# Optimization experiments

Hardware: AMD Instinct MI355X
Metric: run time of the kernel (lower is better)

Reference implementation:

```python
import jax, jax.numpy as jnp
import numpy as np

RADIUS = 0.1
WEIGHT = 0.2
MATMUL_NORM = False


def setup_inputs() -> dict:
    key = jax.random.key(0)
    k1, k2, k3, k4, k5 = jax.random.split(key, 5)
    S, B, Ck, Cv, H, W = 8, 2, 64, 64, 64, 64
    return {
        "memory_keys": jax.random.normal(k1, (S, B, Ck, H, W), jnp.float32),
        "memory_values": jax.random.normal(k2, (S, B, Cv, H, W), jnp.float32),
        "query_query": jax.random.normal(k3, (B, Ck, H, W), jnp.float32),
        "disparity": jax.random.normal(k4, (B, 1, H, W), jnp.float32),
        "sequence_index": jax.random.randint(k5, (B, S, 2), 0, 10, jnp.int32),
    }


def reference(memory_keys, memory_values, query_query, disparity, sequence_index):
    S, B, Ck, H, W = memory_keys.shape
    Cv = memory_values.shape[2]
    HW, SHW = H * W, S * H * W

    # keys: [B, Ck, S*H*W]; queries: [B, H*W, Ck]
    keys = jnp.transpose(memory_keys, (1, 2, 0, 3, 4)).reshape(B, Ck, SHW)
    q = jnp.transpose(query_query.reshape(B, Ck, HW), (0, 2, 1))

    # disparity-based additive mask, vectorized over frames
    weight = WEIGHT / S / H / W
    idx = sequence_index.astype(jnp.float32)
    dist = jnp.sqrt((idx[:, :, 1] - 5.0) ** 2 + (idx[:, :, 0] - 5.0) ** 2)  # [B, S]
    total_disp = dist[:, :, None, None] * disparity  # [B, S, H, W] (disparity [B,1,H,W])
    mask = jnp.where(jnp.abs(total_disp) > RADIUS, weight, 0.0).reshape(B, 1, SHW)

    attn = jnp.einsum("bnc,bcm->bnm", q, keys)  # [B, HW, SHW]
    if MATMUL_NORM:
        attn = attn * (Ck ** -0.5)
    attn = jax.nn.softmax(attn, axis=-1) + mask

    vals = jnp.transpose(memory_values, (1, 0, 3, 4, 2)).reshape(B, SHW, Cv)
    out = jnp.einsum("bnm,bmv->bnv", attn, vals)  # [B, HW, Cv]
    return jnp.transpose(out, (0, 2, 1)).reshape(B, Cv, H, W)
```

## Files before the change

kernel.cpp:

```cpp
#include <hip/hip_runtime.h>
#include <hip/hip_bf16.h>
#include <stdint.h>

#define NS   8
#define NB   2
#define CK   64
#define CV   64
#define HWN  4096
#define SHW  32768
#define RADIUS_ 0.1f
#define MASK_W  6.103515625e-6f

#define TM    32
#define NW    8
#define QS_STR 68
#define P_STR  40
#define SBIAS 24.0f
#define LOG2E 1.4426950408889634f
#define SBIAS2 34.624680981135326f
#define KS    4

#define KT_ELEMS (NS * NB * CK * HWN)
#define KT_BYTES ((size_t)KT_ELEMS * 2)
#define VB_BYTES ((size_t)KT_ELEMS * 2)
#define MASK_OFF (KT_BYTES + VB_BYTES)
#define WS_NEED  (MASK_OFF + (size_t)NB * CV * 4)
#define ONUM_OFF (MASK_OFF + 4096)
#define ONUM_BYTES ((size_t)KS * NB * HWN * CV * 4)
#define ODEN_OFF (ONUM_OFF + ONUM_BYTES)
#define ODEN_BYTES ((size_t)KS * NB * HWN * 4)
#define WS2      (ODEN_OFF + ODEN_BYTES)

typedef __bf16    bf16x8 __attribute__((ext_vector_type(8)));
typedef _Float16  f16x8  __attribute__((ext_vector_type(8)));
typedef float     f32x4  __attribute__((ext_vector_type(4)));
typedef unsigned short u16x8 __attribute__((ext_vector_type(8)));
typedef uint32_t  u32x2 __attribute__((ext_vector_type(2)));
typedef uint32_t  u32x4 __attribute__((ext_vector_type(4)));

__device__ __forceinline__ unsigned short f2bfu(float x) {
  __hip_bfloat16 h = __float2bfloat16(x);
  return __builtin_bit_cast(unsigned short, h);
}
__device__ __forceinline__ bf16x8 ld_bf8_lds(const unsigned short* p) {
  u16x8 u = *(const u16x8*)p;
  return __builtin_bit_cast(bf16x8, u);
}
__device__ __forceinline__ void load_lds16(const void* g, void* l) {
  __builtin_amdgcn_global_load_lds(
      (const __attribute__((address_space(1))) unsigned int*)g,
      (__attribute__((address_space(3))) unsigned int*)l, 16, 0, 0);
}

#define PK_STR 72
__global__ __launch_bounds__(512) void prep_all(
    const float* __restrict__ keys, const float* __restrict__ vals,
    const float* __restrict__ disp, const int* __restrict__ seq,
    _Float16* __restrict__ kT, unsigned short* __restrict__ vbf,
    float* __restrict__ maskadd)
{
  const int t = threadIdx.x;
  const int blk = blockIdx.x;
  if (blk < 256) {
    __shared__ _Float16 lds[256 * PK_STR];
    const int chunk = blk & 15;
    const int s     = (blk >> 4) & 7;
    const int b     = blk >> 7;
    const int hw0   = chunk * 256;
    const int c_st  = t >> 3;
    const int msub  = (t & 7) * 8;

    const float* krow = keys + ((size_t)((s * NB + b) * CK + c_st)) * HWN + hw0;
    #pragma unroll
    for (int r = 0; r < 4; ++r) {
      const int m0 = msub + r * 64;
      f32x4 k0 = *(const f32x4*)(krow + m0);
      f32x4 k1 = *(const f32x4*)(krow + m0 + 4);
      #pragma unroll
      for (int j = 0; j < 4; ++j) {
        lds[(m0 + j)     * PK_STR + c_st] = (_Float16)k0[j];
        lds[(m0 + 4 + j) * PK_STR + c_st] = (_Float16)k1[j];
      }
    }
    __syncthreads();

    _Float16* kout = kT + ((size_t)(b * SHW + s * HWN + hw0)) * CK;
    const int mm = t >> 3, c0 = (t & 7) * 8;
    #pragma unroll
    for (int r2 = 0; r2 < 4; ++r2) {
      const int m = mm + r2 * 64;
      u16x8 v = *(const u16x8*)&lds[m * PK_STR + c0];
      *(u16x8*)(kout + (size_t)m * CK + c0) = v;
    }
  } else {
    const int r = blk - 256;
    const int s = r >> 7;
    const int b = (r >> 6) & 1;
    const int c = r & 63;
    float j0 = (float)seq[(b * NS + s) * 2 + 0];
    float j1 = (float)seq[(b * NS + s) * 2 + 1];
    const float dist = sqrtf((j1 - 5.f) * (j1 - 5.f) + (j0 - 5.f) * (j0 - 5.f));

    const size_t i = (size_t)r * HWN + t * 8;
    const int hw = t * 8;
    f32x4 a  = *(const f32x4*)(vals + i);
    f32x4 bb = *(const f32x4*)(vals + i + 4);
    f32x4 d0 = *(const f32x4*)(disp + (size_t)b * HWN + hw);
    f32x4 d1 = *(const f32x4*)(disp + (size_t)b * HWN + hw + 4);
    u16x8 o;
    float acc = 0.f;
    #pragma unroll
    for (int j = 0; j < 4; ++j) {
      o[j]     = f2bfu(a[j]);
      o[4 + j] = f2bfu(bb[j]);
      if (fabsf(dist * d0[j]) > RADIUS_) acc += a[j];
      if (fabsf(dist * d1[j]) > RADIUS_) acc += bb[j];
    }
    *(u16x8*)(vbf + i) = o;

    #pragma unroll
    for (int m = 32; m >= 1; m >>= 1) acc += __shfl_xor(acc, m);
    __shared__ float red[8];
    if ((t & 63) == 0) red[t >> 6] = acc;
    __syncthreads();
    if (t == 0) {
      float s8 = 0.f;
      #pragma unroll
      for (int j = 0; j < 8; ++j) s8 += red[j];
      atomicAdd(&maskadd[b * CV + c], MASK_W * s8);
    }
  }
}

struct __align__(16) Smem6 {
  union {
    struct {
      _Float16       kbuf[2][128 * 64];
      unsigned short vbuf[2][64 * 128];
    } main;
    struct {
      float obuf[4][32][64];
      float dbuf[4][32];
    } epi;
    float qs[64 * QS_STR];
  };
};

__global__ __launch_bounds__(512, 4) void attn_v6(
    const _Float16* __restrict__ kT,
    const unsigned short* __restrict__ vbf,
    const float* __restrict__ query,
    float* __restrict__ onum,
    float* __restrict__ odenom)
{
  __shared__ Smem6 sm;
  const int t    = threadIdx.x;
  const int w    = t >> 6;
  const int lane = t & 63;
  const int quad = lane >> 4;
  const int l15  = lane & 15;
  const int kq   = w & 3;
  const int rg   = w >> 2;
  const int bidx = blockIdx.x;
  const int xcd  = bidx & 7;
  const int b    = xcd & 1;
  const int ks   = xcd >> 1;
  const int tile = bidx >> 3;
  const int n0   = tile * 64;

  {
    const int qc   = t >> 3;
    const int noff = (t & 7) * 8;
    const int slot = qc ^ ((t & 7) << 2);
    const float* qp = query + (size_t)(b * CK + qc) * HWN + n0 + noff;
    f32x4 q0 = *(const f32x4*)(qp);
    f32x4 q1 = *(const f32x4*)(qp + 4);
    #pragma unroll
    for (int j = 0; j < 4; ++j) {
      sm.qs[(noff + j)     * QS_STR + slot] = q0[j];
      sm.qs[(noff + 4 + j) * QS_STR + slot] = q1[j];
    }
  }
  __syncthreads();
  f16x8 qf[2][2];
  #pragma unroll
  for (int f = 0; f < 2; ++f) {
    const int n  = rg * 32 + f * 16 + l15;
    const int sw = ((n >> 3) & 7) << 2;
    const float* base = &sm.qs[n * QS_STR];
    #pragma unroll
    for (int h = 0; h < 2; ++h) {
      const int c0 = (h * 32 + quad * 8) ^ sw;
      f32x4 a  = *(const f32x4*)(base + c0);
      f32x4 bb = *(const f32x4*)(base + (c0 ^ 4));
      f16x8 q;
      #pragma unroll
      for (int j = 0; j < 4; ++j) {
        q[j]     = (_Float16)(a[j]  * LOG2E);
        q[4 + j] = (_Float16)(bb[j] * LOG2E);
      }
      qf[f][h] = q;
    }
  }
  __syncthreads();

  f32x4 Of[2][4];
  f32x4 Ol[2];
  #pragma unroll
  for (int f = 0; f < 2; ++f) {
    #pragma unroll
    for (int cf = 0; cf < 4; ++cf) Of[f][cf] = (f32x4){0.f, 0.f, 0.f, 0.f};
    Ol[f] = (f32x4){0.f, 0.f, 0.f, 0.f};
  }
  bf16x8 vones;
  #pragma unroll
  for (int i = 0; i < 8; ++i)
    vones[i] = __builtin_bit_cast(__bf16, (unsigned short)0x3F80);

  uint32_t ksrc_off[2];
  int      kldsoff[2];
  uint32_t vsrc_off[2];
  int      vldsoff[2];
  #pragma unroll
  for (int j = 0; j < 2; ++j) {
    const int inst = w * 2 + j;
    const int kl   = inst * 8 + (lane >> 3);
    const int cqs  = lane & 7;
    ksrc_off[j] = (uint32_t)(kl * 128 + ((cqs ^ (kl & 7)) * 16));
    kldsoff[j]  = inst * 1024;
    const int cv  = inst * 4 + (lane >> 4);
    const int chs = (lane & 15) ^ (cv & 7);
    vsrc_off[j] = (uint32_t)(cv * HWN + chs * 8);
    vldsoff[j]  = inst * 1024;
  }
  const char* kgbase = (const char*)(kT + (size_t)b * SHW * CK);
  const int   kbase0 = ks * (SHW / KS);

  {
    const char* kg = kgbase + (size_t)kbase0 * 128;
    load_lds16(kg + ksrc_off[0], (char*)sm.main.kbuf[0] + kldsoff[0]);
    load_lds16(kg + ksrc_off[1], (char*)sm.main.kbuf[0] + kldsoff[1]);
    const int sfrm0 = kbase0 >> 12;
    const unsigned short* vg =
        vbf + (size_t)((sfrm0 * NB + b) * CV) * HWN + (kbase0 & 4095);
    load_lds16(vg + vsrc_off[0], (char*)sm.main.vbuf[0] + vldsoff[0]);
    load_lds16(vg + vsrc_off[1], (char*)sm.main.vbuf[0] + vldsoff[1]);
  }

  for (int it = 0; it < 64; ++it) {
    const int cur  = it & 1;
    const int key0 = kbase0 + it * 128;

    __syncthreads();

    if (it < 63) {
      const int keyn = key0 + 128;
      const char* kg = kgbase + (size_t)keyn * 128;
      load_lds16(kg + ksrc_off[0], (char*)sm.main.kbuf[cur ^ 1] + kldsoff[0]);
      load_lds16(kg + ksrc_off[1], (char*)sm.main.kbuf[cur ^ 1] + kldsoff[1]);
      const int sfrmn = keyn >> 12;
      const unsigned short* vg =
          vbf + (size_t)((sfrmn * NB + b) * CV) * HWN + (keyn & 4095);
      load_lds16(vg + vsrc_off[0], (char*)sm.main.vbuf[cur ^ 1] + vldsoff[0]);
      load_lds16(vg + vsrc_off[1], (char*)sm.main.vbuf[cur ^ 1] + vldsoff[1]);
    }

    f16x8 kf[2][2];
    #pragma unroll
    for (int g = 0; g < 2; ++g) {
      const int kl  = kq * 32 + g * 16 + l15;
      const int swz = kl & 7;
      const _Float16* kb = &sm.main.kbuf[cur][kl * 64];
      #pragma unroll
      for (int h = 0; h < 2; ++h) {
        const int slot = (h * 4 + quad) ^ swz;
        kf[g][h] = *(const f16x8*)(kb + slot * 8);
      }
    }

    bf16x8 vf[4];
    {
      const int c0 = kq * 4 + (quad >> 1);
      const int ho = (quad & 1) * 4;
      #pragma unroll
      for (int cf = 0; cf < 4; ++cf) {
        const int cv  = cf * 16 + l15;
        const int swz = cv & 7;
        const unsigned short* row = &sm.main.vbuf[cur][cv * 128];
        u32x2 lo = *(const u32x2*)(row + ((c0       ^ swz) * 8) + ho);
        u32x2 hi = *(const u32x2*)(row + (((c0 + 2) ^ swz) * 8) + ho);
        vf[cf] = __builtin_bit_cast(bf16x8, (u32x4){lo.x, lo.y, hi.x, hi.y});
      }
    }

    f32x4 sf[2][2];
    #pragma unroll
    for (int g = 0; g < 2; ++g)
      #pragma unroll
      for (int f = 0; f < 2; ++f) {
        f32x4 acc = (f32x4){-SBIAS2, -SBIAS2, -SBIAS2, -SBIAS2};
        acc = __builtin_amdgcn_mfma_f32_16x16x32_f16(kf[g][0], qf[f][0], acc, 0, 0, 0);
        acc = __builtin_amdgcn_mfma_f32_16x16x32_f16(kf[g][1], qf[f][1], acc, 0, 0, 0);
        sf[g][f] = acc;
      }

    #pragma unroll
    for (int f = 0; f < 2; ++f) {
      uint32_t pk[2][2];
      #pragma unroll
      for (int g = 0; g < 2; ++g) {
        float e0 = __builtin_amdgcn_exp2f(sf[g][f][0]);
        float e1 = __builtin_amdgcn_exp2f(sf[g][f][1]);
        float e2 = __builtin_amdgcn_exp2f(sf[g][f][2]);
        float e3 = __builtin_amdgcn_exp2f(sf[g][f][3]);
        pk[g][0] = __builtin_amdgcn_perm(__builtin_bit_cast(uint32_t, e1),
                                         __builtin_bit_cast(uint32_t, e0),
                                         0x07060302u);
        pk[g][1] = __builtin_amdgcn_perm(__builtin_bit_cast(uint32_t, e3),
                                         __builtin_bit_cast(uint32_t, e2),
                                         0x07060302u);
      }
      bf16x8 pf = __builtin_bit_cast(bf16x8,
          (u32x4){pk[0][0], pk[0][1], pk[1][0], pk[1][1]});

      #pragma unroll
      for (int cf = 0; cf < 4; ++cf)
        Of[f][cf] = __builtin_amdgcn_mfma_f32_16x16x32_bf16(pf, vf[cf], Of[f][cf], 0, 0, 0);
      Ol[f] = __builtin_amdgcn_mfma_f32_16x16x32_bf16(pf, vones, Ol[f], 0, 0, 0);
    }
  }

  __syncthreads();

  #pragma unroll
  for (int phase = 0; phase < 2; ++phase) {
    if (rg == phase) {
      #pragma unroll
      for (int f = 0; f < 2; ++f)
        #pragma unroll
        for (int r = 0; r < 4; ++r) {
          const int row = f * 16 + quad * 4 + r;
          if (l15 == 0) sm.epi.dbuf[kq][row] = Ol[f][r];
          #pragma unroll
          for (int cf = 0; cf < 4; ++cf)
            sm.epi.obuf[kq][row][cf * 16 + l15] = Of[f][cf][r];
        }
    }
    __syncthreads();
    {
      const int row = t >> 4;
      const int v4  = (t & 15) * 4;
      f32x4 acc = *(const f32x4*)&sm.epi.obuf[0][row][v4];
      #pragma unroll
      for (int q = 1; q < 4; ++q)
        acc += *(const f32x4*)&sm.epi.obuf[q][row][v4];
      *(f32x4*)&onum[((size_t)(ks * NB + b) * HWN + n0 + phase * 32 + row) * CV + v4] = acc;
      if (t < 32) {
        float d = sm.epi.dbuf[0][t] + sm.epi.dbuf[1][t] +
                  sm.epi.dbuf[2][t] + sm.epi.dbuf[3][t];
        odenom[(size_t)(ks * NB + b) * HWN + n0 + phase * 32 + t] = d;
      }
    }
    __syncthreads();
  }
}

__global__ __launch_bounds__(256) void finalize_k(
    const float* __restrict__ onum, const float* __restrict__ odenom,
    const float* __restrict__ maskadd, float* __restrict__ out)
{
  __shared__ float tile[64][68];
  __shared__ float dinv[64];
  __shared__ float ml[64];
  const int t   = threadIdx.x;
  const int b   = blockIdx.x >> 6;
  const int hw0 = (blockIdx.x & 63) * 64;

  #pragma unroll
  for (int pass = 0; pass < 4; ++pass) {
    const int row = pass * 16 + (t >> 4);
    const int v4  = (t & 15) * 4;
    f32x4 acc = (f32x4){0.f, 0.f, 0.f, 0.f};
    #pragma unroll
    for (int ks = 0; ks < KS; ++ks)
      acc += *(const f32x4*)&onum[((size_t)(ks * NB + b) * HWN + hw0 + row) * CV + v4];
    *(f32x4*)&tile[row][v4] = acc;
  }
  if (t < 64) {
    float d = 0.f;
    #pragma unroll
    for (int ks = 0; ks < KS; ++ks)
      d += odenom[(size_t)(ks * NB + b) * HWN + hw0 + t];
    dinv[t] = 1.f / fmaxf(d, 1e-30f);
  }
  if (t >= 64 && t < 128) ml[t - 64] = maskadd[b * CV + (t - 64)];
  __syncthreads();

  #pragma unroll
  for (int pass = 0; pass < 4; ++pass) {
    const int v   = pass * 16 + (t >> 4);
    const int hw4 = (t & 15) * 4;
    f32x4 o;
    #pragma unroll
    for (int j = 0; j < 4; ++j)
      o[j] = tile[hw4 + j][v] * dinv[hw4 + j] + ml[v];
    *(f32x4*)&out[((size_t)(b * CV + v)) * HWN + hw0 + hw4] = o;
  }
}

struct __align__(16) SmemF {
  union {
    float qs[TM * QS_STR];
    unsigned short p[NW][2][16 * P_STR];
    struct {
      float obuf[NW][TM][CV];
      float lbuf[NW][TM];
    } epi;
  };
};

__global__ __launch_bounds__(512) void attn_fast(
    const _Float16* __restrict__ kT, const unsigned short* __restrict__ vbf,
    const float* __restrict__ query, const float* __restrict__ maskadd,
    float* __restrict__ out)
{
  __shared__ SmemF sm;
  const int t    = threadIdx.x;
  const int w    = t >> 6;
  const int lane = t & 63;
  const int quad = lane >> 4;
  const int l15  = lane & 15;
  const int bidx = blockIdx.x;
  const int b    = bidx & 1;
  const int n0   = ((bidx >> 1) & 127) * TM;

  if (t < 256) {
    const int qc   = t >> 2;
    const int noff = (t & 3) * 8;
    const int slot = qc ^ ((t & 3) << 2);
    const float* qp = query + (size_t)(b * CK + qc) * HWN + n0 + noff;
    f32x4 q0 = *(const f32x4*)(qp);
    f32x4 q1 = *(const f32x4*)(qp + 4);
    #pragma unroll
    for (int j = 0; j < 4; ++j) {
      sm.qs[(noff + j)     * QS_STR + slot] = q0[j];
      sm.qs[(noff + 4 + j) * QS_STR + slot] = q1[j];
    }
  }
  __syncthreads();
  f16x8 qf[2][2];
  #pragma unroll
  for (int f = 0; f < 2; ++f) {
    const int n  = f * 16 + l15;
    const int sw = ((n >> 3) & 7) << 2;
    const float* base = &sm.qs[n * QS_STR];
    #pragma unroll
    for (int h = 0; h < 2; ++h) {
      const int c0 = (h * 32 + quad * 8) ^ sw;
      f32x4 a  = *(const f32x4*)(base + c0);
      f32x4 bb = *(const f32x4*)(base + (c0 ^ 4));
      f16x8 q;
      #pragma unroll
      for (int j = 0; j < 4; ++j) { q[j] = (_Float16)a[j]; q[4 + j] = (_Float16)bb[j]; }
      qf[f][h] = q;
    }
  }
  __syncthreads();

  f32x4 Of[2][4];
  f32x4 Ol[2];
  #pragma unroll
  for (int f = 0; f < 2; ++f) {
    #pragma unroll
    for (int cf = 0; cf < 4; ++cf) Of[f][cf] = (f32x4){0.f, 0.f, 0.f, 0.f};
    Ol[f] = (f32x4){0.f, 0.f, 0.f, 0.f};
  }
  bf16x8 vones;
  #pragma unroll
  for (int i = 0; i < 8; ++i)
    vones[i] = __builtin_bit_cast(__bf16, (unsigned short)0x3F80);

  const _Float16* kbase = kT + (size_t)b * SHW * CK;

  for (int it = 0; it < SHW / 256; ++it) {
    const int key0 = it * 256 + w * 32;
    f16x8 kf[2][2];
    #pragma unroll
    for (int g = 0; g < 2; ++g)
      #pragma unroll
      for (int h = 0; h < 2; ++h)
        kf[g][h] = *(const f16x8*)(kbase +
            (size_t)(key0 + g * 16 + l15) * CK + h * 32 + quad * 8);

    const int s   = it >> 4;
    const int hwv = (it & 15) * 256 + w * 32 + quad * 8;
    bf16x8 vf[4];
    #pragma unroll
    for (int cf = 0; cf < 4; ++cf)
      vf[cf] = ld_bf8_lds(vbf +
          ((size_t)((s * NB + b) * CV + cf * 16 + l15)) * HWN + hwv);

    f32x4 sfv[2][2];
    #pragma unroll
    for (int f = 0; f < 2; ++f)
      #pragma unroll
      for (int g = 0; g < 2; ++g) {
        f32x4 acc = (f32x4){0.f, 0.f, 0.f, 0.f};
        acc = __builtin_amdgcn_mfma_f32_16x16x32_f16(qf[f][0], kf[g][0], acc, 0, 0, 0);
        acc = __builtin_amdgcn_mfma_f32_16x16x32_f16(qf[f][1], kf[g][1], acc, 0, 0, 0);
        sfv[f][g] = acc;
      }

    #pragma unroll
    for (int f = 0; f < 2; ++f)
      #pragma unroll
      for (int g = 0; g < 2; ++g)
        #pragma unroll
        for (int r = 0; r < 4; ++r)
          sfv[f][g][r] = __expf(sfv[f][g][r] - SBIAS);

    #pragma unroll
    for (int f = 0; f < 2; ++f)
      #pragma unroll
      for (int g = 0; g < 2; ++g)
        #pragma unroll
        for (int r = 0; r < 4; ++r)
          sm.p[w][f][(quad * 4 + r) * P_STR + g * 16 + l15] = f2bfu(sfv[f][g][r]);
    asm volatile("s_waitcnt lgkmcnt(0)" ::: "memory");
    bf16x8 pf[2];
    #pragma unroll
    for (int f = 0; f < 2; ++f)
      pf[f] = ld_bf8_lds(&sm.p[w][f][l15 * P_STR + quad * 8]);

    #pragma unroll
    for (int f = 0; f < 2; ++f) {
      #pragma unroll
      for (int cf = 0; cf < 4; ++cf)
        Of[f][cf] = __builtin_amdgcn_mfma_f32_16x16x32_bf16(pf[f], vf[cf], Of[f][cf], 0, 0, 0);
      Ol[f] = __builtin_amdgcn_mfma_f32_16x16x32_bf16(pf[f], vones, Ol[f], 0, 0, 0);
    }
  }

  __syncthreads();
  #pragma unroll
  for (int f = 0; f < 2; ++f)
    #pragma unroll
    for (int r = 0; r < 4; ++r) {
      const int row = f * 16 + quad * 4 + r;
      if (l15 == 0) sm.epi.lbuf[w][row] = Ol[f][r];
      #pragma unroll
      for (int cf = 0; cf < 4; ++cf)
        sm.epi.obuf[w][row][cf * 16 + l15] = Of[f][cf][r];
    }
  __syncthreads();
  {
    const int n   = t & 31;
    const int vhi = t >> 5;
    float denom = 0.f;
    #pragma unroll
    for (int ww = 0; ww < NW; ++ww) denom += sm.epi.lbuf[ww][n];
    const float inv = 1.f / fmaxf(denom, 1e-30f);
    #pragma unroll
    for (int g = 0; g < 4; ++g) {
      const int v = vhi + 16 * g;
      float num = 0.f;
      #pragma unroll
      for (int ww = 0; ww < NW; ++ww) num += sm.epi.obuf[ww][n][v];
      out[((size_t)(b * CV + v)) * HWN + n0 + n] = num * inv + maskadd[b * CV + v];
    }
  }
}

extern "C" void kernel_launch(void* const* d_in, const int* in_sizes, int n_in,
                              void* d_out, int out_size, void* d_ws, size_t ws_size,
                              hipStream_t stream) {
  const float* keys  = (const float*)d_in[0];
  const float* vals  = (const float*)d_in[1];
  const float* query = (const float*)d_in[2];
  const float* disp  = (const float*)d_in[3];
  const int*   seq   = (const int*)d_in[4];
  float*       out   = (float*)d_out;

  _Float16*       kT   = (_Float16*)d_ws;
  unsigned short* vbf  = (unsigned short*)((char*)d_ws + KT_BYTES);
  float*          mask = (float*)((char*)d_ws + MASK_OFF);

  hipMemsetAsync(mask, 0, (size_t)NB * CV * 4, stream);
  prep_all<<<256 + NB * NS * CV, 512, 0, stream>>>(keys, vals, disp, seq, kT, vbf, mask);

  if (ws_size >= WS2) {
    float* onum   = (float*)((char*)d_ws + ONUM_OFF);
    float* odenom = (float*)((char*)d_ws + ODEN_OFF);
    attn_v6<<<NB * 64 * KS, 512, 0, stream>>>(kT, vbf, query, onum, odenom);
    finalize_k<<<NB * (HWN / 64), 256, 0, stream>>>(onum, odenom, mask, out);
  } else {
    attn_fast<<<NB * (HWN / TM), 512, 0, stream>>>(kT, vbf, query, mask, out);
  }
}
```

Before: 172.3 us.

## Pre-permute bf16 values for single LDS loads and drop mask memset/atomics

The prep kernel now writes the bf16 value rows in a permuted 8-element chunk order. This lets the attention kernel fetch each MFMA operand with one 16-byte LDS read instead of two 8-byte reads. The mask contribution is now stored per frame into a partial buffer and summed in the finalize/epilogue. That removes the hipMemsetAsync launch and the global atomics. The fallback kernel is adjusted to read the permuted layout with split loads.

```diff
diff --git a/kernel.cpp b/kernel.cpp
--- a/kernel.cpp
+++ b/kernel.cpp
@@ -23,9 +23,9 @@
 #define KT_ELEMS (NS * NB * CK * HWN)
 #define KT_BYTES ((size_t)KT_ELEMS * 2)
 #define VB_BYTES ((size_t)KT_ELEMS * 2)
-#define MASK_OFF (KT_BYTES + VB_BYTES)
-#define WS_NEED  (MASK_OFF + (size_t)NB * CV * 4)
-#define ONUM_OFF (MASK_OFF + 4096)
+#define MASKP_OFF (KT_BYTES + VB_BYTES)
+#define WS_NEED  (MASKP_OFF + 4096)
+#define ONUM_OFF (MASKP_OFF + 4096)
 #define ONUM_BYTES ((size_t)KS * NB * HWN * CV * 4)
 #define ODEN_OFF (ONUM_OFF + ONUM_BYTES)
 #define ODEN_BYTES ((size_t)KS * NB * HWN * 4)
@@ -52,12 +52,13 @@
       (__attribute__((address_space(3))) unsigned int*)l, 16, 0, 0);
 }
 
+
 #define PK_STR 72
 __global__ __launch_bounds__(512) void prep_all(
     const float* __restrict__ keys, const float* __restrict__ vals,
     const float* __restrict__ disp, const int* __restrict__ seq,
     _Float16* __restrict__ kT, unsigned short* __restrict__ vbf,
-    float* __restrict__ maskadd)
+    float* __restrict__ maskpart)
 {
   const int t = threadIdx.x;
   const int blk = blockIdx.x;
@@ -116,10 +117,18 @@
       if (fabsf(dist * d0[j]) > RADIUS_) acc += a[j];
       if (fabsf(dist * d1[j]) > RADIUS_) acc += bb[j];
     }
-    *(u16x8*)(vbf + i) = o;
-
-    #pragma unroll
-    for (int m = 32; m >= 1; m >>= 1) acc += __shfl_xor(acc, m);
+    {
+      const int m  = t & 3;
+      const int pa = ((2 * m) & 3) * 2 + (m >> 1);
+      const int pb = ((2 * m + 1) & 3) * 2 + (m >> 1);
+      unsigned short* rowp = vbf + (size_t)r * HWN + (t >> 2) * 32;
+      u32x4 wv = __builtin_bit_cast(u32x4, o);
+      *(u32x2*)(rowp + pa * 4) = (u32x2){wv.x, wv.y};
+      *(u32x2*)(rowp + pb * 4) = (u32x2){wv.z, wv.w};
+    }
+
+    #pragma unroll
+    for (int m2 = 32; m2 >= 1; m2 >>= 1) acc += __shfl_xor(acc, m2);
     __shared__ float red[8];
     if ((t & 63) == 0) red[t >> 6] = acc;
     __syncthreads();
@@ -127,7 +136,7 @@
       float s8 = 0.f;
       #pragma unroll
       for (int j = 0; j < 8; ++j) s8 += red[j];
-      atomicAdd(&maskadd[b * CV + c], MASK_W * s8);
+      maskpart[(b * CV + c) * NS + s] = MASK_W * s8;
     }
   }
 }
@@ -280,16 +289,12 @@
 
     bf16x8 vf[4];
     {
-      const int c0 = kq * 4 + (quad >> 1);
-      const int ho = (quad & 1) * 4;
+      const int ch = kq * 4 + quad;
       #pragma unroll
       for (int cf = 0; cf < 4; ++cf) {
         const int cv  = cf * 16 + l15;
         const int swz = cv & 7;
-        const unsigned short* row = &sm.main.vbuf[cur][cv * 128];
-        u32x2 lo = *(const u32x2*)(row + ((c0       ^ swz) * 8) + ho);
-        u32x2 hi = *(const u32x2*)(row + (((c0 + 2) ^ swz) * 8) + ho);
-        vf[cf] = __builtin_bit_cast(bf16x8, (u32x4){lo.x, lo.y, hi.x, hi.y});
+        vf[cf] = ld_bf8_lds(&sm.main.vbuf[cur][cv * 128 + ((ch ^ swz) << 3)]);
       }
     }
 
@@ -367,7 +372,7 @@
 
 __global__ __launch_bounds__(256) void finalize_k(
     const float* __restrict__ onum, const float* __restrict__ odenom,
-    const float* __restrict__ maskadd, float* __restrict__ out)
+    const float* __restrict__ maskpart, float* __restrict__ out)
 {
   __shared__ float tile[64][68];
   __shared__ float dinv[64];
@@ -393,7 +398,12 @@
       d += odenom[(size_t)(ks * NB + b) * HWN + hw0 + t];
     dinv[t] = 1.f / fmaxf(d, 1e-30f);
   }
-  if (t >= 64 && t < 128) ml[t - 64] = maskadd[b * CV + (t - 64)];
+  if (t >= 64 && t < 128) {
+    float m = 0.f;
+    #pragma unroll
+    for (int s = 0; s < NS; ++s) m += maskpart[(b * CV + (t - 64)) * NS + s];
+    ml[t - 64] = m;
+  }
   __syncthreads();
 
   #pragma unroll
@@ -421,7 +431,7 @@
 
 __global__ __launch_bounds__(512) void attn_fast(
     const _Float16* __restrict__ kT, const unsigned short* __restrict__ vbf,
-    const float* __restrict__ query, const float* __restrict__ maskadd,
+    const float* __restrict__ query, const float* __restrict__ maskpart,
     float* __restrict__ out)
 {
   __shared__ SmemF sm;
@@ -493,12 +503,18 @@
             (size_t)(key0 + g * 16 + l15) * CK + h * 32 + quad * 8);
 
     const int s   = it >> 4;
-    const int hwv = (it & 15) * 256 + w * 32 + quad * 8;
+    const int hwg = (it & 15) * 256 + w * 32;
+    const int pa  = ((2 * quad) & 3) * 2 + (quad >> 1);
+    const int pb  = ((2 * quad + 1) & 3) * 2 + (quad >> 1);
     bf16x8 vf[4];
     #pragma unroll
-    for (int cf = 0; cf < 4; ++cf)
-      vf[cf] = ld_bf8_lds(vbf +
-          ((size_t)((s * NB + b) * CV + cf * 16 + l15)) * HWN + hwv);
+    for (int cf = 0; cf < 4; ++cf) {
+      const unsigned short* rowp = vbf +
+          ((size_t)((s * NB + b) * CV + cf * 16 + l15)) * HWN + hwg;
+      u32x2 lo = *(const u32x2*)(rowp + pa * 4);
+      u32x2 hi = *(const u32x2*)(rowp + pb * 4);
+      vf[cf] = __builtin_bit_cast(bf16x8, (u32x4){lo.x, lo.y, hi.x, hi.y});
+    }
 
     f32x4 sfv[2][2];
     #pragma unroll
@@ -566,7 +582,10 @@
       float num = 0.f;
       #pragma unroll
       for (int ww = 0; ww < NW; ++ww) num += sm.epi.obuf[ww][n][v];
-      out[((size_t)(b * CV + v)) * HWN + n0 + n] = num * inv + maskadd[b * CV + v];
+      float mlv = 0.f;
+      #pragma unroll
+      for (int s = 0; s < NS; ++s) mlv += maskpart[(b * CV + v) * NS + s];
+      out[((size_t)(b * CV + v)) * HWN + n0 + n] = num * inv + mlv;
     }
   }
 }
@@ -581,19 +600,19 @@
   const int*   seq   = (const int*)d_in[4];
   float*       out   = (float*)d_out;
 
-  _Float16*       kT   = (_Float16*)d_ws;
-  unsigned short* vbf  = (unsigned short*)((char*)d_ws + KT_BYTES);
-  float*          mask = (float*)((char*)d_ws + MASK_OFF);
-
-  hipMemsetAsync(mask, 0, (size_t)NB * CV * 4, stream);
-  prep_all<<<256 + NB * NS * CV, 512, 0, stream>>>(keys, vals, disp, seq, kT, vbf, mask);
+  _Float16*       kT    = (_Float16*)d_ws;
+  unsigned short* vbf   = (unsigned short*)((char*)d_ws + KT_BYTES);
+  float*          maskp = (float*)((char*)d_ws + MASKP_OFF);
+
+  prep_all<<<256 + NB * NS * CV, 512, 0, stream>>>(keys, vals, disp, seq,
+                                                   kT, vbf, maskp);
 
   if (ws_size >= WS2) {
     float* onum   = (float*)((char*)d_ws + ONUM_OFF);
     float* odenom = (float*)((char*)d_ws + ODEN_OFF);
     attn_v6<<<NB * 64 * KS, 512, 0, stream>>>(kT, vbf, query, onum, odenom);
-    finalize_k<<<NB * (HWN / 64), 256, 0, stream>>>(onum, odenom, mask, out);
+    finalize_k<<<NB * (HWN / 64), 256, 0, stream>>>(onum, odenom, maskp, out);
   } else {
-    attn_fast<<<NB * (HWN / TM), 512, 0, stream>>>(kT, vbf, query, mask, out);
-  }
-}
+    attn_fast<<<NB * (HWN / TM), 512, 0, stream>>>(kT, vbf, query, maskp, out);
+  }
+}
```

Result: faster. 162.9 us (-5.5%).
